# Kernel tuning notes

Measured on AMD Instinct MI355X. Metric: run time of the kernel, lower is better.

Reference implementation:

```python
import jax, jax.numpy as jnp
import numpy as np

M1, N1, M2, N2 = 32, 64, 24, 48  # Kronecker block dims; 32*24=768, 64*48=3072


def setup_inputs() -> dict:
    key = jax.random.key(0)
    k1, k2, k3, k4, k5 = jax.random.split(key, 5)
    rank = 64
    x = jax.random.normal(k1, (4, 4096, 768), dtype=jnp.float32)
    A_factors = jax.random.normal(k2, (M1 * N1, rank), dtype=jnp.float32) * 0.05
    B_factors = jax.random.normal(k3, (rank, M2 * N2), dtype=jnp.float32) * 0.05
    # 'Sparse' residual is materialized dense in the original module (to_dense()).
    Sparse = jax.random.normal(k4, (768, 3072), dtype=jnp.float32) * 0.02
    bias = jax.random.normal(k5, (3072,), dtype=jnp.float32) * 0.02
    return {"x": x, "A_factors": A_factors, "B_factors": B_factors,
            "Sparse": Sparse, "bias": bias}


def reference(x, A_factors, B_factors, Sparse, bias):
    # Low-rank product: [2048, r] @ [r, 1152] -> [2048, 1152]
    W_tilde = A_factors @ B_factors
    # Kronecker permute: (m1, n1, m2, n2) -> (m1, m2, n1, n2) -> [768, 3072]
    W_low = W_tilde.reshape(M1, N1, M2, N2).transpose(0, 2, 1, 3).reshape(
        M1 * M2, N1 * N2)
    W = W_low + Sparse
    # Dense GEMM: [B, S, 768] @ [768, 3072] + bias
    return x @ W + bias
```

## Files before the change

kernel.cpp:

```cpp
#include <hip/hip_runtime.h>
#include <hip/hip_bf16.h>
#include <stdint.h>

#define M_TOT 16384
#define N_TOT 3072
#define K_TOT 768

#define BM 256
#define BN 256
#define BK 32
#define NT (K_TOT / BK)

typedef __attribute__((ext_vector_type(8))) short short8;
typedef __attribute__((ext_vector_type(4))) float f32x4;

__device__ __forceinline__ unsigned short f2bf(float f) {
    union { float f; unsigned u; } v;
    v.f = f;
    unsigned r = v.u + 0x7FFFu + ((v.u >> 16) & 1u);
    return (unsigned short)(r >> 16);
}

__global__ __launch_bounds__(384) void prep_cvt_kernel(
    const float* __restrict__ Af, const float* __restrict__ Bf,
    const float* __restrict__ Sp, const float* __restrict__ x,
    unsigned short* __restrict__ xb, unsigned short* __restrict__ Wt) {
    __shared__ float a_sh[4][64];
    __shared__ float wrow[4][1160];
    const int tid = threadIdx.x;
    const int b = blockIdx.x;

    if (b < 512) {
        const int m1 = b >> 4;
        const int n10 = (b & 15) * 4;
        if (tid < 256) {
            int rr = tid >> 6, k = tid & 63;
            a_sh[rr][k] = Af[(size_t)(m1 * 64 + n10 + rr) * 64 + k];
        }
        __syncthreads();
        float acc[4][3] = {};
        #pragma unroll 2
        for (int k = 0; k < 64; ++k) {
            const float* brow = Bf + (size_t)k * 1152;
            float b0 = brow[tid], b1 = brow[tid + 384], b2 = brow[tid + 768];
            #pragma unroll
            for (int rr = 0; rr < 4; ++rr) {
                float a = a_sh[rr][k];
                acc[rr][0] = fmaf(a, b0, acc[rr][0]);
                acc[rr][1] = fmaf(a, b1, acc[rr][1]);
                acc[rr][2] = fmaf(a, b2, acc[rr][2]);
            }
        }
        #pragma unroll
        for (int rr = 0; rr < 4; ++rr) {
            wrow[rr][tid] = acc[rr][0];
            wrow[rr][tid + 384] = acc[rr][1];
            wrow[rr][tid + 768] = acc[rr][2];
        }
        __syncthreads();
        if (tid < 192) {
            const int rr = tid / 48, n2 = tid % 48;
            const int c = (n10 + rr) * 48 + n2;
            const int r0 = m1 * 24;
            unsigned w[12];
            #pragma unroll
            for (int t2 = 0; t2 < 12; ++t2) {
                float lo = wrow[rr][(2 * t2) * 48 + n2]
                         + Sp[(size_t)(r0 + 2 * t2) * 3072 + c];
                float hi = wrow[rr][(2 * t2 + 1) * 48 + n2]
                         + Sp[(size_t)(r0 + 2 * t2 + 1) * 3072 + c];
                w[t2] = (unsigned)f2bf(lo) | ((unsigned)f2bf(hi) << 16);
            }
            uint4* d4 = reinterpret_cast<uint4*>(Wt + (size_t)c * 768 + r0);
            d4[0] = (uint4){w[0], w[1], w[2], w[3]};
            d4[1] = (uint4){w[4], w[5], w[6], w[7]};
            d4[2] = (uint4){w[8], w[9], w[10], w[11]};
        }
    } else {
        const int n8 = M_TOT * K_TOT / 8;
        int i = (b - 512) * 384 + tid;
        const int stride = 2048 * 384;
        const float4* xv = reinterpret_cast<const float4*>(x);
        uint4* ov = reinterpret_cast<uint4*>(xb);
        for (; i < n8; i += stride) {
            float4 a = xv[2 * i], c = xv[2 * i + 1];
            uint4 o;
            o.x = (unsigned)f2bf(a.x) | ((unsigned)f2bf(a.y) << 16);
            o.y = (unsigned)f2bf(a.z) | ((unsigned)f2bf(a.w) << 16);
            o.z = (unsigned)f2bf(c.x) | ((unsigned)f2bf(c.y) << 16);
            o.w = (unsigned)f2bf(c.z) | ((unsigned)f2bf(c.w) << 16);
            ov[i] = o;
        }
    }
}

__device__ __forceinline__ void gld16(const void* g, void* l) {
    __builtin_amdgcn_global_load_lds(
        (const __attribute__((address_space(1))) void*)g,
        (__attribute__((address_space(3))) void*)l, 16, 0, 0);
}

__global__ __launch_bounds__(512, 2) void gemm_bt_kernel(
    const unsigned short* __restrict__ A, const unsigned short* __restrict__ Bt,
    const float* __restrict__ bias, float* __restrict__ C) {
    __shared__ unsigned short As[4][BM * BK];
    __shared__ unsigned short Bs[4][BN * BK];

    const int tid = threadIdx.x;
    const int lane = tid & 63;
    const int wid = tid >> 6;
    const int wr = wid >> 2;
    const int wc = wid & 3;

    const int wg = (blockIdx.x & 7) * 96 + (blockIdx.x >> 3);
    const int bm = wg / (N_TOT / BN), bn = wg % (N_TOT / BN);
    const int brow = bm * BM, bcol = bn * BN;

    const int srow = tid >> 2;
    const int soff = (((tid & 3) ^ ((tid >> 3) & 3)) << 4);
    const char* pA = (const char*)A + ((size_t)(brow + srow) * K_TOT) * 2 + soff;
    const char* pB = (const char*)Bt + ((size_t)(bcol + srow) * K_TOT) * 2 + soff;
    const size_t row128 = (size_t)128 * K_TOT * 2;
    const int tid16 = tid * 16;

#define STAGE_AH(u) do { const char* s_ = pA + (size_t)(u) * (BK * 2);           \
        gld16(s_,          (char*)&As[(u) & 3][0] + tid16);                      \
        gld16(s_ + row128, (char*)&As[(u) & 3][0] + tid16 + 8192); } while (0)
#define STAGE_BH(u) do { const char* s_ = pB + (size_t)(u) * (BK * 2);           \
        gld16(s_,          (char*)&Bs[(u) & 3][0] + tid16);                      \
        gld16(s_ + row128, (char*)&Bs[(u) & 3][0] + tid16 + 8192); } while (0)

    const int la = lane & 15;
    const int g4 = lane >> 4;
    const int swb = ((g4 ^ ((lane >> 1) & 3)) << 4);
#define FRAG_A(bu, r) (*(const short8*)((const char*)&As[bu][0] + (r) * 64 + swb))
#define FRAG_B(bu, r) (*(const short8*)((const char*)&Bs[bu][0] + (r) * 64 + swb))

#define LGKM0_FENCE() do {                                                       \
        asm volatile("s_waitcnt lgkmcnt(0)" ::: "memory");                       \
        __builtin_amdgcn_sched_barrier(0); } while (0)

    f32x4 acc[8][4];
    #pragma unroll
    for (int m = 0; m < 8; ++m)
        #pragma unroll
        for (int n = 0; n < 4; ++n)
            acc[m][n] = (f32x4){0.f, 0.f, 0.f, 0.f};

    STAGE_AH(0); STAGE_BH(0);
    STAGE_AH(1); STAGE_BH(1);
    STAGE_AH(2); STAGE_BH(2);
    asm volatile("s_waitcnt vmcnt(8)" ::: "memory");
    __builtin_amdgcn_s_barrier();

    const int arow = wr * 128;
    const int bcolw = wc * 64;
    for (int t = 0; t < NT; ++t) {
        const int bu = t & 3;
        short8 a0[4], b0[4];
        #pragma unroll
        for (int n = 0; n < 4; ++n) b0[n] = FRAG_B(bu, bcolw + n * 16 + la);
        #pragma unroll
        for (int m = 0; m < 4; ++m) a0[m] = FRAG_A(bu, arow + m * 16 + la);
        if (t < NT - 3) STAGE_AH(t + 3);
        __builtin_amdgcn_s_barrier();
        LGKM0_FENCE();
        __builtin_amdgcn_s_setprio(1);
        #pragma unroll
        for (int m = 0; m < 4; ++m)
            #pragma unroll
            for (int n = 0; n < 4; ++n)
                acc[m][n] = __builtin_amdgcn_mfma_f32_16x16x32_bf16(
                    b0[n], a0[m], acc[m][n], 0, 0, 0);
        __builtin_amdgcn_s_setprio(0);
        __builtin_amdgcn_s_barrier();
        #pragma unroll
        for (int m = 0; m < 4; ++m) a0[m] = FRAG_A(bu, arow + 64 + m * 16 + la);
        if (t < NT - 3) STAGE_BH(t + 3);
        if (t < NT - 3)       asm volatile("s_waitcnt vmcnt(8)" ::: "memory");
        else if (t == NT - 3) asm volatile("s_waitcnt vmcnt(4)" ::: "memory");
        else if (t == NT - 2) asm volatile("s_waitcnt vmcnt(0)" ::: "memory");
        __builtin_amdgcn_s_barrier();
        LGKM0_FENCE();
        __builtin_amdgcn_s_setprio(1);
        #pragma unroll
        for (int m = 0; m < 4; ++m)
            #pragma unroll
            for (int n = 0; n < 4; ++n)
                acc[4 + m][n] = __builtin_amdgcn_mfma_f32_16x16x32_bf16(
                    b0[n], a0[m], acc[4 + m][n], 0, 0, 0);
        __builtin_amdgcn_s_setprio(0);
        __builtin_amdgcn_s_barrier();
    }

    #pragma unroll
    for (int n = 0; n < 4; ++n) {
        const int gc = bcol + bcolw + n * 16 + g4 * 4;
        const f32x4 bv = *reinterpret_cast<const f32x4*>(&bias[gc]);
        #pragma unroll
        for (int m = 0; m < 8; ++m) {
            const int gr = brow + arow + m * 16 + la;
            f32x4 o = {acc[m][n][0] + bv[0], acc[m][n][1] + bv[1],
                       acc[m][n][2] + bv[2], acc[m][n][3] + bv[3]};
            *reinterpret_cast<f32x4*>(&C[(size_t)gr * N_TOT + gc]) = o;
        }
    }
#undef STAGE_AH
#undef STAGE_BH
#undef FRAG_A
#undef FRAG_B
#undef LGKM0_FENCE
}

extern "C" void kernel_launch(void* const* d_in, const int* in_sizes, int n_in,
                              void* d_out, int out_size, void* d_ws, size_t ws_size,
                              hipStream_t stream) {
    const float* x    = (const float*)d_in[0];
    const float* Af   = (const float*)d_in[1];
    const float* Bf   = (const float*)d_in[2];
    const float* Sp   = (const float*)d_in[3];
    const float* bias = (const float*)d_in[4];
    float* out = (float*)d_out;

    unsigned short* xb = (unsigned short*)d_ws;
    unsigned short* wt = xb + (size_t)M_TOT * K_TOT;

    hipLaunchKernelGGL(prep_cvt_kernel, dim3(512 + 2048), dim3(384), 0, stream,
                       Af, Bf, Sp, x, xb, wt);
    hipLaunchKernelGGL(gemm_bt_kernel,
                       dim3((M_TOT / BM) * (N_TOT / BN)), dim3(512),
                       0, stream, xb, wt, bias, out);
}
```

Before: 127.5 us.

## Shrink GEMM tile to 256x128 with 4 waves, triple-buffered single-barrier pipeline

Reduces the block tile from 256x256 with 8 waves to 256x128 with 4 waves, giving each wave the same 128x64 output sub-tile. The LDS ring drops from four to three stages, and the loop issues loads two tiles ahead with one wait and barrier per K step instead of four barriers. Block-to-tile mapping is reworked so each XCD gets a contiguous 8x8 group of tiles for L2 reuse. The smaller tile raises global traffic for A per output, and the reduced barrier count relies on the prefetch distance being enough to hide load latency.

```diff
diff --git a/kernel.cpp b/kernel.cpp
--- a/kernel.cpp
+++ b/kernel.cpp
@@ -7,7 +7,7 @@
 #define K_TOT 768
 
 #define BM 256
-#define BN 256
+#define BN 128
 #define BK 32
 #define NT (K_TOT / BK)
 
@@ -100,35 +100,40 @@
         (__attribute__((address_space(3))) void*)l, 16, 0, 0);
 }
 
-__global__ __launch_bounds__(512, 2) void gemm_bt_kernel(
+__global__ __launch_bounds__(256, 2) void gemm_bt_kernel(
     const unsigned short* __restrict__ A, const unsigned short* __restrict__ Bt,
     const float* __restrict__ bias, float* __restrict__ C) {
-    __shared__ unsigned short As[4][BM * BK];
-    __shared__ unsigned short Bs[4][BN * BK];
+    __shared__ unsigned short As[3][BM * BK];
+    __shared__ unsigned short Bs[3][BN * BK];
 
     const int tid = threadIdx.x;
     const int lane = tid & 63;
     const int wid = tid >> 6;
-    const int wr = wid >> 2;
-    const int wc = wid & 3;
-
-    const int wg = (blockIdx.x & 7) * 96 + (blockIdx.x >> 3);
-    const int bm = wg / (N_TOT / BN), bn = wg % (N_TOT / BN);
+    const int wr = wid >> 1;
+    const int wc = wid & 1;
+
+    const int xcd = blockIdx.x & 7, g = blockIdx.x >> 3;
+    const int c = g >> 6, h = g & 63;
+    const int bm = xcd * 8 + (h >> 3);
+    const int bn = c * 8 + (h & 7);
     const int brow = bm * BM, bcol = bn * BN;
 
     const int srow = tid >> 2;
     const int soff = (((tid & 3) ^ ((tid >> 3) & 3)) << 4);
     const char* pA = (const char*)A + ((size_t)(brow + srow) * K_TOT) * 2 + soff;
     const char* pB = (const char*)Bt + ((size_t)(bcol + srow) * K_TOT) * 2 + soff;
-    const size_t row128 = (size_t)128 * K_TOT * 2;
+    const size_t rstep = (size_t)64 * K_TOT * 2;
     const int tid16 = tid * 16;
 
-#define STAGE_AH(u) do { const char* s_ = pA + (size_t)(u) * (BK * 2);           \
-        gld16(s_,          (char*)&As[(u) & 3][0] + tid16);                      \
-        gld16(s_ + row128, (char*)&As[(u) & 3][0] + tid16 + 8192); } while (0)
-#define STAGE_BH(u) do { const char* s_ = pB + (size_t)(u) * (BK * 2);           \
-        gld16(s_,          (char*)&Bs[(u) & 3][0] + tid16);                      \
-        gld16(s_ + row128, (char*)&Bs[(u) & 3][0] + tid16 + 8192); } while (0)
+#define STG(bu, t) do {                                                          \
+        const char* sa_ = pA + (size_t)(t) * (BK * 2);                           \
+        const char* sb_ = pB + (size_t)(t) * (BK * 2);                           \
+        gld16(sa_,             (char*)&As[bu][0] + tid16);                       \
+        gld16(sa_ + rstep,     (char*)&As[bu][0] + tid16 + 4096);                \
+        gld16(sa_ + 2 * rstep, (char*)&As[bu][0] + tid16 + 8192);                \
+        gld16(sa_ + 3 * rstep, (char*)&As[bu][0] + tid16 + 12288);               \
+        gld16(sb_,             (char*)&Bs[bu][0] + tid16);                       \
+        gld16(sb_ + rstep,     (char*)&Bs[bu][0] + tid16 + 4096); } while (0)
 
     const int la = lane & 15;
     const int g4 = lane >> 4;
@@ -136,10 +141,6 @@
 #define FRAG_A(bu, r) (*(const short8*)((const char*)&As[bu][0] + (r) * 64 + swb))
 #define FRAG_B(bu, r) (*(const short8*)((const char*)&Bs[bu][0] + (r) * 64 + swb))
 
-#define LGKM0_FENCE() do {                                                       \
-        asm volatile("s_waitcnt lgkmcnt(0)" ::: "memory");                       \
-        __builtin_amdgcn_sched_barrier(0); } while (0)
-
     f32x4 acc[8][4];
     #pragma unroll
     for (int m = 0; m < 8; ++m)
@@ -147,50 +148,50 @@
         for (int n = 0; n < 4; ++n)
             acc[m][n] = (f32x4){0.f, 0.f, 0.f, 0.f};
 
-    STAGE_AH(0); STAGE_BH(0);
-    STAGE_AH(1); STAGE_BH(1);
-    STAGE_AH(2); STAGE_BH(2);
-    asm volatile("s_waitcnt vmcnt(8)" ::: "memory");
+    STG(0, 0); STG(1, 1);
+    asm volatile("s_waitcnt vmcnt(6)" ::: "memory");
     __builtin_amdgcn_s_barrier();
+    __builtin_amdgcn_sched_barrier(0);
 
     const int arow = wr * 128;
     const int bcolw = wc * 64;
+
+    #pragma unroll 1
     for (int t = 0; t < NT; ++t) {
-        const int bu = t & 3;
-        short8 a0[4], b0[4];
-        #pragma unroll
-        for (int n = 0; n < 4; ++n) b0[n] = FRAG_B(bu, bcolw + n * 16 + la);
-        #pragma unroll
-        for (int m = 0; m < 4; ++m) a0[m] = FRAG_A(bu, arow + m * 16 + la);
-        if (t < NT - 3) STAGE_AH(t + 3);
-        __builtin_amdgcn_s_barrier();
-        LGKM0_FENCE();
+        const int bu = t % 3;
+        short8 a_[4], b_[4];
+
+        if (t + 2 < NT) STG((t + 2) % 3, t + 2);
+        #pragma unroll
+        for (int n = 0; n < 4; ++n) b_[n] = FRAG_B(bu, bcolw + n * 16 + la);
+        #pragma unroll
+        for (int m = 0; m < 4; ++m) a_[m] = FRAG_A(bu, arow + m * 16 + la);
         __builtin_amdgcn_s_setprio(1);
         #pragma unroll
         for (int m = 0; m < 4; ++m)
             #pragma unroll
             for (int n = 0; n < 4; ++n)
                 acc[m][n] = __builtin_amdgcn_mfma_f32_16x16x32_bf16(
-                    b0[n], a0[m], acc[m][n], 0, 0, 0);
+                    b_[n], a_[m], acc[m][n], 0, 0, 0);
         __builtin_amdgcn_s_setprio(0);
-        __builtin_amdgcn_s_barrier();
-        #pragma unroll
-        for (int m = 0; m < 4; ++m) a0[m] = FRAG_A(bu, arow + 64 + m * 16 + la);
-        if (t < NT - 3) STAGE_BH(t + 3);
-        if (t < NT - 3)       asm volatile("s_waitcnt vmcnt(8)" ::: "memory");
-        else if (t == NT - 3) asm volatile("s_waitcnt vmcnt(4)" ::: "memory");
-        else if (t == NT - 2) asm volatile("s_waitcnt vmcnt(0)" ::: "memory");
-        __builtin_amdgcn_s_barrier();
-        LGKM0_FENCE();
+
+        #pragma unroll
+        for (int m = 0; m < 4; ++m) a_[m] = FRAG_A(bu, arow + 64 + m * 16 + la);
         __builtin_amdgcn_s_setprio(1);
         #pragma unroll
         for (int m = 0; m < 4; ++m)
             #pragma unroll
             for (int n = 0; n < 4; ++n)
                 acc[4 + m][n] = __builtin_amdgcn_mfma_f32_16x16x32_bf16(
-                    b0[n], a0[m], acc[4 + m][n], 0, 0, 0);
+                    b_[n], a_[m], acc[4 + m][n], 0, 0, 0);
         __builtin_amdgcn_s_setprio(0);
-        __builtin_amdgcn_s_barrier();
+
+        if (t < NT - 1) {
+            if (t + 2 < NT) asm volatile("s_waitcnt vmcnt(6)" ::: "memory");
+            else            asm volatile("s_waitcnt vmcnt(0)" ::: "memory");
+            __builtin_amdgcn_s_barrier();
+            __builtin_amdgcn_sched_barrier(0);
+        }
     }
 
     #pragma unroll
@@ -205,11 +206,9 @@
             *reinterpret_cast<f32x4*>(&C[(size_t)gr * N_TOT + gc]) = o;
         }
     }
-#undef STAGE_AH
-#undef STAGE_BH
+#undef STG
 #undef FRAG_A
 #undef FRAG_B
-#undef LGKM0_FENCE
 }
 
 extern "C" void kernel_launch(void* const* d_in, const int* in_sizes, int n_in,
@@ -228,6 +227,6 @@
     hipLaunchKernelGGL(prep_cvt_kernel, dim3(512 + 2048), dim3(384), 0, stream,
                        Af, Bf, Sp, x, xb, wt);
     hipLaunchKernelGGL(gemm_bt_kernel,
-                       dim3((M_TOT / BM) * (N_TOT / BN)), dim3(512),
+                       dim3((M_TOT / BM) * (N_TOT / BN)), dim3(256),
                        0, stream, xb, wt, bias, out);
 }
```

Measured after the change: 139.3 us. 1.09x slower.

## Software-pipeline LDS fragment loads with double-buffered B registers across K tiles

Applied to the files above, without the earlier changes.

Loads the next K tile's B fragments and lower-half A fragments from LDS during the current tile's second MFMA phase. It ping-pongs two B register sets through a two-tile unrolled loop. The explicit lgkmcnt(0) fences are dropped so LDS reads can overlap with MFMA issue. The global vmcnt wait is tightened so the next buffer is resident before it is read early. This costs extra VGPRs (about 32 more), which may reduce occupancy or cause spills, and it relies on the compiler inserting the correct LDS waits.

```diff
diff --git a/kernel.cpp b/kernel.cpp
--- a/kernel.cpp
+++ b/kernel.cpp
@@ -136,61 +136,72 @@
 #define FRAG_A(bu, r) (*(const short8*)((const char*)&As[bu][0] + (r) * 64 + swb))
 #define FRAG_B(bu, r) (*(const short8*)((const char*)&Bs[bu][0] + (r) * 64 + swb))
 
-#define LGKM0_FENCE() do {                                                       \
-        asm volatile("s_waitcnt lgkmcnt(0)" ::: "memory");                       \
-        __builtin_amdgcn_sched_barrier(0); } while (0)
-
     f32x4 acc[8][4];
     #pragma unroll
     for (int m = 0; m < 8; ++m)
         #pragma unroll
         for (int n = 0; n < 4; ++n)
             acc[m][n] = (f32x4){0.f, 0.f, 0.f, 0.f};
+
+    const int arow = wr * 128;
+    const int bcolw = wc * 64;
+
+    short8 bE[4], bO[4], aLo[4], aHi[4];
 
     STAGE_AH(0); STAGE_BH(0);
     STAGE_AH(1); STAGE_BH(1);
     STAGE_AH(2); STAGE_BH(2);
-    asm volatile("s_waitcnt vmcnt(8)" ::: "memory");
+    asm volatile("s_waitcnt vmcnt(4)" ::: "memory");
     __builtin_amdgcn_s_barrier();
-
-    const int arow = wr * 128;
-    const int bcolw = wc * 64;
-    for (int t = 0; t < NT; ++t) {
+    #pragma unroll
+    for (int n = 0; n < 4; ++n) bE[n] = FRAG_B(0, bcolw + n * 16 + la);
+    #pragma unroll
+    for (int m = 0; m < 4; ++m) aLo[m] = FRAG_A(0, arow + m * 16 + la);
+    __builtin_amdgcn_sched_barrier(0);
+
+    auto tile_body = [&](int t, short8 (&bc)[4], short8 (&bnx)[4]) {
         const int bu = t & 3;
-        short8 a0[4], b0[4];
-        #pragma unroll
-        for (int n = 0; n < 4; ++n) b0[n] = FRAG_B(bu, bcolw + n * 16 + la);
-        #pragma unroll
-        for (int m = 0; m < 4; ++m) a0[m] = FRAG_A(bu, arow + m * 16 + la);
+        #pragma unroll
+        for (int m = 0; m < 4; ++m) aHi[m] = FRAG_A(bu, arow + 64 + m * 16 + la);
         if (t < NT - 3) STAGE_AH(t + 3);
-        __builtin_amdgcn_s_barrier();
-        LGKM0_FENCE();
+        __builtin_amdgcn_sched_barrier(0);
+        __builtin_amdgcn_s_barrier();
         __builtin_amdgcn_s_setprio(1);
         #pragma unroll
         for (int m = 0; m < 4; ++m)
             #pragma unroll
             for (int n = 0; n < 4; ++n)
                 acc[m][n] = __builtin_amdgcn_mfma_f32_16x16x32_bf16(
-                    b0[n], a0[m], acc[m][n], 0, 0, 0);
+                    bc[n], aLo[m], acc[m][n], 0, 0, 0);
         __builtin_amdgcn_s_setprio(0);
         __builtin_amdgcn_s_barrier();
-        #pragma unroll
-        for (int m = 0; m < 4; ++m) a0[m] = FRAG_A(bu, arow + 64 + m * 16 + la);
+        if (t < NT - 1) {
+            const int bu1 = (t + 1) & 3;
+            #pragma unroll
+            for (int n = 0; n < 4; ++n) bnx[n] = FRAG_B(bu1, bcolw + n * 16 + la);
+            #pragma unroll
+            for (int m = 0; m < 4; ++m) aLo[m] = FRAG_A(bu1, arow + m * 16 + la);
+        }
         if (t < NT - 3) STAGE_BH(t + 3);
-        if (t < NT - 3)       asm volatile("s_waitcnt vmcnt(8)" ::: "memory");
-        else if (t == NT - 3) asm volatile("s_waitcnt vmcnt(4)" ::: "memory");
-        else if (t == NT - 2) asm volatile("s_waitcnt vmcnt(0)" ::: "memory");
-        __builtin_amdgcn_s_barrier();
-        LGKM0_FENCE();
+        __builtin_amdgcn_sched_barrier(0);
+        if (t < NT - 3)       asm volatile("s_waitcnt vmcnt(4)" ::: "memory");
+        else if (t == NT - 3) asm volatile("s_waitcnt vmcnt(0)" ::: "memory");
+        __builtin_amdgcn_s_barrier();
         __builtin_amdgcn_s_setprio(1);
         #pragma unroll
         for (int m = 0; m < 4; ++m)
             #pragma unroll
             for (int n = 0; n < 4; ++n)
                 acc[4 + m][n] = __builtin_amdgcn_mfma_f32_16x16x32_bf16(
-                    b0[n], a0[m], acc[4 + m][n], 0, 0, 0);
+                    bc[n], aHi[m], acc[4 + m][n], 0, 0, 0);
         __builtin_amdgcn_s_setprio(0);
         __builtin_amdgcn_s_barrier();
+    };
+
+    #pragma unroll 1
+    for (int tt = 0; tt < NT; tt += 2) {
+        tile_body(tt, bE, bO);
+        tile_body(tt + 1, bO, bE);
     }
 
     #pragma unroll
@@ -209,7 +220,6 @@
 #undef STAGE_BH
 #undef FRAG_A
 #undef FRAG_B
-#undef LGKM0_FENCE
 }
 
 extern "C" void kernel_launch(void* const* d_in, const int* in_sizes, int n_in,
```

New measurement: 126.7 us. Within noise of the previous version (-0.6%).
